# Optimization experiments

Measured on AMD Instinct MI355X. Metric: run time of the kernel, lower is better.

Reference implementation:

```python
import jax, jax.numpy as jnp
import numpy as np

B, C, L = 16, 256, 4096
P, Q = 100, 20


def setup_inputs() -> dict:
    key = jax.random.key(0)
    k1, k2, k3, k4 = jax.random.split(key, 4)
    X = jax.random.normal(k1, (B, C, L), dtype=jnp.float32)
    projections = jax.random.normal(k2, (P, C), dtype=jnp.float32)
    # min < max per projection. Projected values ~ N(0, sqrt(C)), so scale ~ sqrt(C).
    scale = jnp.sqrt(jnp.float32(C))
    min_vals = -scale * (1.0 + jax.random.uniform(k3, (P,), dtype=jnp.float32))
    max_vals = scale * (1.0 + jax.random.uniform(k4, (P,), dtype=jnp.float32))
    return {"X": X, "projections": projections, "min_vals": min_vals, "max_vals": max_vals}


def reference(X, projections, min_vals, max_vals):
    # conv1d with kernel size 1 == per-position projection: [B,C,L] x [P,C] -> [B,P,L]
    a = jnp.einsum('bcl,pc->bpl', X, projections)
    # all quantile thresholds at once: thr[p,q] = min + (max-min)*(q+1)/(Q+1)
    fracs = (jnp.arange(1, Q + 1, dtype=jnp.float32)) / jnp.float32(Q + 1)  # [Q]
    thr = min_vals[:, None] + (max_vals - min_vals)[:, None] * fracs[None, :]  # [P,Q]
    # set[b,p,l,q] = a[b,p,l] < thr[p,q]
    set_ = (a[:, :, :, None] < thr[None, :, None, :]).astype(jnp.float32)  # [B,P,L,Q]
    cdf = jnp.mean(set_, axis=2)  # [B,P,Q]
    # transpose(2,1) -> [B,L,P,Q]; reshape -> [B,L,P*Q]; transpose(2,1) -> [B,P*Q,L]
    set_out = jnp.transpose(set_, (0, 2, 1, 3)).reshape(B, L, P * Q)
    set_out = jnp.transpose(set_out, (0, 2, 1))  # [B, P*Q, L]
    cdf_out = cdf.reshape(B, P * Q)
    return (cdf_out, set_out)
```

## Files before the change

### kernel.cpp

```cpp
#include <hip/hip_runtime.h>

#define Bsz 16
#define Cc  256
#define Ll  4096
#define Pp  100
#define Qq  20
#define PQ  (Pp * Qq)

#define LTILE 1024
#define NLT   (Ll / LTILE)
#define GP    10
#define NPG   (Pp / GP)

typedef float f32x4 __attribute__((ext_vector_type(4)));

__global__ __launch_bounds__(256) void csf_main(
    const float* __restrict__ X,
    const float* __restrict__ proj,
    const float* __restrict__ mn,
    const float* __restrict__ mx,
    float* __restrict__ cdf,
    float* __restrict__ set_out) {
    const int lt  = blockIdx.x;
    const int pg  = blockIdx.y;
    const int b   = blockIdx.z;
    const int tid = threadIdx.x;
    const int l0  = lt * LTILE + tid * 4;
    const int p0  = __builtin_amdgcn_readfirstlane(pg * GP);

    const float* Xb = X + (size_t)b * Cc * Ll + l0;

    float acc[GP][4];
#pragma unroll
    for (int i = 0; i < GP; i++)
#pragma unroll
        for (int k = 0; k < 4; k++) acc[i][k] = 0.0f;

#pragma unroll 4
    for (int c = 0; c < Cc; c++) {
        const f32x4 x = *(const f32x4*)(Xb + (size_t)c * Ll);
#pragma unroll
        for (int i = 0; i < GP; i++) {
            const float w = proj[(size_t)(p0 + i) * Cc + c];
            acc[i][0] = __builtin_fmaf(x.x, w, acc[i][0]);
            acc[i][1] = __builtin_fmaf(x.y, w, acc[i][1]);
            acc[i][2] = __builtin_fmaf(x.z, w, acc[i][2]);
            acc[i][3] = __builtin_fmaf(x.w, w, acc[i][3]);
        }
    }

    float fr[Qq];
#pragma unroll
    for (int q = 0; q < Qq; q++) fr[q] = __fdiv_rn((float)(q + 1), 21.0f);

    float* ob = set_out + (size_t)b * PQ * Ll + l0;
    const bool lane0 = ((tid & 63) == 0);

#pragma unroll 1
    for (int i = 0; i < GP; i++) {
        const int p = p0 + i;
        const float mnp = mn[p];
        const float mxp = mx[p];
        const float d = __fsub_rn(mxp, mnp);
#pragma unroll
        for (int q = 0; q < Qq; q++) {
            const float thr = __fadd_rn(mnp, __fmul_rn(d, fr[q]));
            const bool b0 = acc[i][0] < thr;
            const bool b1 = acc[i][1] < thr;
            const bool b2 = acc[i][2] < thr;
            const bool b3 = acc[i][3] < thr;
            f32x4 o;
            o.x = b0 ? 1.0f : 0.0f;
            o.y = b1 ? 1.0f : 0.0f;
            o.z = b2 ? 1.0f : 0.0f;
            o.w = b3 ? 1.0f : 0.0f;
            __builtin_nontemporal_store(o, (f32x4*)(ob + (size_t)(p * Qq + q) * Ll));
            const int cnt = __popcll(__ballot(b0)) + __popcll(__ballot(b1))
                          + __popcll(__ballot(b2)) + __popcll(__ballot(b3));
            if (lane0) {
                atomicAdd(&cdf[(size_t)b * PQ + p * Qq + q],
                          (float)cnt * (1.0f / (float)Ll));
            }
        }
    }
}

extern "C" void kernel_launch(void* const* d_in, const int* in_sizes, int n_in,
                              void* d_out, int out_size, void* d_ws, size_t ws_size,
                              hipStream_t stream) {
    const float* X    = (const float*)d_in[0];
    const float* proj = (const float*)d_in[1];
    const float* mn   = (const float*)d_in[2];
    const float* mx   = (const float*)d_in[3];

    float* cdf     = (float*)d_out;
    float* set_out = cdf + (size_t)Bsz * PQ;

    (void)hipMemsetAsync(cdf, 0, (size_t)Bsz * PQ * sizeof(float), stream);

    dim3 grid(NLT, NPG, Bsz);
    csf_main<<<grid, 256, 0, stream>>>(X, proj, mn, mx, cdf, set_out);
}
```

Baseline: 606.4 us.

## Split projection and thresholding into two kernels, staging projections in output buffer

Projection now runs in its own kernel where each thread keeps all 100 projection accumulators and reads X exactly once, with 8-channel software prefetch. The old kernel re-read X once per group of 10 projections. The projected values go to the first quantile slot of the output, and a second kernel reads them back to write the thresholded masks and cdf. In exchange it adds an extra round trip through global memory, a second launch, and high register pressure from the 100 accumulators, which may lower occupancy or cause spills.

```diff
diff --git a/kernel.cpp b/kernel.cpp
--- a/kernel.cpp
+++ b/kernel.cpp
@@ -7,97 +7,113 @@
 #define Qq  20
 #define PQ  (Pp * Qq)
 
-#define LTILE 1024
-#define NLT   (Ll / LTILE)
-#define GP    10
-#define NPG   (Pp / GP)
-
 typedef float f32x4 __attribute__((ext_vector_type(4)));
 
-__global__ __launch_bounds__(256) void csf_main(
+
+__global__ __launch_bounds__(256) void csf_proj(
     const float* __restrict__ X,
     const float* __restrict__ proj,
+    float* __restrict__ set_out) {
+  const int l = blockIdx.x * 256 + threadIdx.x;
+  const int b = blockIdx.y;
+  const float* Xb = X + (size_t)b * Cc * Ll + l;
+
+  float acc[Pp];
+#pragma unroll
+  for (int p = 0; p < Pp; p++) acc[p] = 0.0f;
+
+  float x[8];
+#pragma unroll
+  for (int j = 0; j < 8; j++) x[j] = Xb[(size_t)j * Ll];
+
+#pragma unroll 1
+  for (int cc = 0; cc < Cc; cc += 8) {
+    float xn[8];
+    const bool more = (cc + 8 < Cc);
+    if (more) {
+#pragma unroll
+      for (int j = 0; j < 8; j++) xn[j] = Xb[(size_t)(cc + 8 + j) * Ll];
+    }
+#pragma unroll
+    for (int p = 0; p < Pp; p++) {
+      const float* pr = proj + (size_t)p * Cc + cc;
+#pragma unroll
+      for (int j = 0; j < 8; j++)
+        acc[p] = __builtin_fmaf(x[j], pr[j], acc[p]);
+    }
+    if (more) {
+#pragma unroll
+      for (int j = 0; j < 8; j++) x[j] = xn[j];
+    }
+  }
+
+  float* ob = set_out + (size_t)b * PQ * Ll + l;
+#pragma unroll
+  for (int p = 0; p < Pp; p++)
+    ob[(size_t)p * Qq * Ll] = acc[p];
+}
+
+__global__ __launch_bounds__(256) void csf_thresh(
     const float* __restrict__ mn,
     const float* __restrict__ mx,
     float* __restrict__ cdf,
     float* __restrict__ set_out) {
-    const int lt  = blockIdx.x;
-    const int pg  = blockIdx.y;
-    const int b   = blockIdx.z;
-    const int tid = threadIdx.x;
-    const int l0  = lt * LTILE + tid * 4;
-    const int p0  = __builtin_amdgcn_readfirstlane(pg * GP);
+  const int lt  = blockIdx.x;
+  const int p   = blockIdx.y;
+  const int b   = blockIdx.z;
+  const int tid = threadIdx.x;
+  const int l0  = lt * 1024 + tid * 4;
 
-    const float* Xb = X + (size_t)b * Cc * Ll + l0;
+  float* ob = set_out + (size_t)b * PQ * Ll + (size_t)p * Qq * Ll + l0;
+  const f32x4 a = *(const f32x4*)ob;
 
-    float acc[GP][4];
+  const float mnp = mn[p];
+  const float mxp = mx[p];
+  const float d   = __fsub_rn(mxp, mnp);
+
+  const float FR[Qq] = {
+     1.0f/21.0f,  2.0f/21.0f,  3.0f/21.0f,  4.0f/21.0f,  5.0f/21.0f,
+     6.0f/21.0f,  7.0f/21.0f,  8.0f/21.0f,  9.0f/21.0f, 10.0f/21.0f,
+    11.0f/21.0f, 12.0f/21.0f, 13.0f/21.0f, 14.0f/21.0f, 15.0f/21.0f,
+    16.0f/21.0f, 17.0f/21.0f, 18.0f/21.0f, 19.0f/21.0f, 20.0f/21.0f };
+
+  const bool lane0 = ((tid & 63) == 0);
+  float* cp = cdf + (size_t)b * PQ + (size_t)p * Qq;
+
 #pragma unroll
-    for (int i = 0; i < GP; i++)
-#pragma unroll
-        for (int k = 0; k < 4; k++) acc[i][k] = 0.0f;
-
-#pragma unroll 4
-    for (int c = 0; c < Cc; c++) {
-        const f32x4 x = *(const f32x4*)(Xb + (size_t)c * Ll);
-#pragma unroll
-        for (int i = 0; i < GP; i++) {
-            const float w = proj[(size_t)(p0 + i) * Cc + c];
-            acc[i][0] = __builtin_fmaf(x.x, w, acc[i][0]);
-            acc[i][1] = __builtin_fmaf(x.y, w, acc[i][1]);
-            acc[i][2] = __builtin_fmaf(x.z, w, acc[i][2]);
-            acc[i][3] = __builtin_fmaf(x.w, w, acc[i][3]);
-        }
+  for (int q = 0; q < Qq; q++) {
+    const float thr = __fadd_rn(mnp, __fmul_rn(d, FR[q]));
+    const bool b0 = a.x < thr;
+    const bool b1 = a.y < thr;
+    const bool b2 = a.z < thr;
+    const bool b3 = a.w < thr;
+    f32x4 o;
+    o.x = b0 ? 1.0f : 0.0f;
+    o.y = b1 ? 1.0f : 0.0f;
+    o.z = b2 ? 1.0f : 0.0f;
+    o.w = b3 ? 1.0f : 0.0f;
+    __builtin_nontemporal_store(o, (f32x4*)(ob + (size_t)q * Ll));
+    const int cnt = __popcll(__ballot(b0)) + __popcll(__ballot(b1))
+                  + __popcll(__ballot(b2)) + __popcll(__ballot(b3));
+    if (lane0) {
+      atomicAdd(cp + q, (float)cnt * (1.0f / (float)Ll));
     }
-
-    float fr[Qq];
-#pragma unroll
-    for (int q = 0; q < Qq; q++) fr[q] = __fdiv_rn((float)(q + 1), 21.0f);
-
-    float* ob = set_out + (size_t)b * PQ * Ll + l0;
-    const bool lane0 = ((tid & 63) == 0);
-
-#pragma unroll 1
-    for (int i = 0; i < GP; i++) {
-        const int p = p0 + i;
-        const float mnp = mn[p];
-        const float mxp = mx[p];
-        const float d = __fsub_rn(mxp, mnp);
-#pragma unroll
-        for (int q = 0; q < Qq; q++) {
-            const float thr = __fadd_rn(mnp, __fmul_rn(d, fr[q]));
-            const bool b0 = acc[i][0] < thr;
-            const bool b1 = acc[i][1] < thr;
-            const bool b2 = acc[i][2] < thr;
-            const bool b3 = acc[i][3] < thr;
-            f32x4 o;
-            o.x = b0 ? 1.0f : 0.0f;
-            o.y = b1 ? 1.0f : 0.0f;
-            o.z = b2 ? 1.0f : 0.0f;
-            o.w = b3 ? 1.0f : 0.0f;
-            __builtin_nontemporal_store(o, (f32x4*)(ob + (size_t)(p * Qq + q) * Ll));
-            const int cnt = __popcll(__ballot(b0)) + __popcll(__ballot(b1))
-                          + __popcll(__ballot(b2)) + __popcll(__ballot(b3));
-            if (lane0) {
-                atomicAdd(&cdf[(size_t)b * PQ + p * Qq + q],
-                          (float)cnt * (1.0f / (float)Ll));
-            }
-        }
-    }
+  }
 }
 
 extern "C" void kernel_launch(void* const* d_in, const int* in_sizes, int n_in,
                               void* d_out, int out_size, void* d_ws, size_t ws_size,
                               hipStream_t stream) {
-    const float* X    = (const float*)d_in[0];
-    const float* proj = (const float*)d_in[1];
-    const float* mn   = (const float*)d_in[2];
-    const float* mx   = (const float*)d_in[3];
+  const float* X    = (const float*)d_in[0];
+  const float* proj = (const float*)d_in[1];
+  const float* mn   = (const float*)d_in[2];
+  const float* mx   = (const float*)d_in[3];
 
-    float* cdf     = (float*)d_out;
-    float* set_out = cdf + (size_t)Bsz * PQ;
+  float* cdf     = (float*)d_out;
+  float* set_out = cdf + (size_t)Bsz * PQ;
 
-    (void)hipMemsetAsync(cdf, 0, (size_t)Bsz * PQ * sizeof(float), stream);
+  (void)hipMemsetAsync(cdf, 0, (size_t)Bsz * PQ * sizeof(float), stream);
 
-    dim3 grid(NLT, NPG, Bsz);
-    csf_main<<<grid, 256, 0, stream>>>(X, proj, mn, mx, cdf, set_out);
+  csf_proj<<<dim3(Ll / 256, Bsz), 256, 0, stream>>>(X, proj, set_out);
+  csf_thresh<<<dim3(Ll / 1024, Pp, Bsz), 256, 0, stream>>>(mn, mx, cdf, set_out);
 }
```

Result: slower. 871.7 us (+43.7%).

## Stage X tiles in shared memory and split projections across waves per block

Applied to the files above, without the earlier changes.

The kernel now handles one batch and a 64-position tile per block, staging 64-channel chunks of X in LDS. Each of its four waves computes 25 projections for all 64 positions, so X is read from global memory once rather than ten times across projection groups. Each lane now holds one position instead of four. Stores therefore become scalar (4-byte) nontemporal writes, and there are four times as many ballots and atomics per output element. The output write of roughly 524 MB dominates, so the narrower stores could hurt write efficiency.

```diff
diff --git a/kernel.cpp b/kernel.cpp
--- a/kernel.cpp
+++ b/kernel.cpp
@@ -7,97 +7,95 @@
 #define Qq  20
 #define PQ  (Pp * Qq)
 
-#define LTILE 1024
-#define NLT   (Ll / LTILE)
-#define GP    10
-#define NPG   (Pp / GP)
+#define LT   64
+#define CCH  64
+#define PW   25
 
 typedef float f32x4 __attribute__((ext_vector_type(4)));
 
-__global__ __launch_bounds__(256) void csf_main(
+__global__ __launch_bounds__(256, 4) void csf_fused(
     const float* __restrict__ X,
     const float* __restrict__ proj,
     const float* __restrict__ mn,
     const float* __restrict__ mx,
     float* __restrict__ cdf,
     float* __restrict__ set_out) {
-    const int lt  = blockIdx.x;
-    const int pg  = blockIdx.y;
-    const int b   = blockIdx.z;
-    const int tid = threadIdx.x;
-    const int l0  = lt * LTILE + tid * 4;
-    const int p0  = __builtin_amdgcn_readfirstlane(pg * GP);
+  __shared__ float xs[CCH][LT];
 
-    const float* Xb = X + (size_t)b * Cc * Ll + l0;
+  const int b    = blockIdx.y;
+  const int l0   = blockIdx.x * LT;
+  const int tid  = threadIdx.x;
+  const int wave = tid >> 6;
+  const int lane = tid & 63;
+  const int p0   = __builtin_amdgcn_readfirstlane(wave * PW);
 
-    float acc[GP][4];
+  const int lsub = (tid & 15) * 4;
+  const int crow = tid >> 4;
+  const float* Xg = X + (size_t)b * Cc * Ll + l0 + lsub;
+
+  float acc[PW];
 #pragma unroll
-    for (int i = 0; i < GP; i++)
-#pragma unroll
-        for (int k = 0; k < 4; k++) acc[i][k] = 0.0f;
-
-#pragma unroll 4
-    for (int c = 0; c < Cc; c++) {
-        const f32x4 x = *(const f32x4*)(Xb + (size_t)c * Ll);
-#pragma unroll
-        for (int i = 0; i < GP; i++) {
-            const float w = proj[(size_t)(p0 + i) * Cc + c];
-            acc[i][0] = __builtin_fmaf(x.x, w, acc[i][0]);
-            acc[i][1] = __builtin_fmaf(x.y, w, acc[i][1]);
-            acc[i][2] = __builtin_fmaf(x.z, w, acc[i][2]);
-            acc[i][3] = __builtin_fmaf(x.w, w, acc[i][3]);
-        }
-    }
-
-    float fr[Qq];
-#pragma unroll
-    for (int q = 0; q < Qq; q++) fr[q] = __fdiv_rn((float)(q + 1), 21.0f);
-
-    float* ob = set_out + (size_t)b * PQ * Ll + l0;
-    const bool lane0 = ((tid & 63) == 0);
+  for (int i = 0; i < PW; i++) acc[i] = 0.0f;
 
 #pragma unroll 1
-    for (int i = 0; i < GP; i++) {
-        const int p = p0 + i;
-        const float mnp = mn[p];
-        const float mxp = mx[p];
-        const float d = __fsub_rn(mxp, mnp);
+  for (int ch = 0; ch < Cc; ch += CCH) {
+    if (ch) __syncthreads();
 #pragma unroll
-        for (int q = 0; q < Qq; q++) {
-            const float thr = __fadd_rn(mnp, __fmul_rn(d, fr[q]));
-            const bool b0 = acc[i][0] < thr;
-            const bool b1 = acc[i][1] < thr;
-            const bool b2 = acc[i][2] < thr;
-            const bool b3 = acc[i][3] < thr;
-            f32x4 o;
-            o.x = b0 ? 1.0f : 0.0f;
-            o.y = b1 ? 1.0f : 0.0f;
-            o.z = b2 ? 1.0f : 0.0f;
-            o.w = b3 ? 1.0f : 0.0f;
-            __builtin_nontemporal_store(o, (f32x4*)(ob + (size_t)(p * Qq + q) * Ll));
-            const int cnt = __popcll(__ballot(b0)) + __popcll(__ballot(b1))
-                          + __popcll(__ballot(b2)) + __popcll(__ballot(b3));
-            if (lane0) {
-                atomicAdd(&cdf[(size_t)b * PQ + p * Qq + q],
-                          (float)cnt * (1.0f / (float)Ll));
-            }
-        }
+    for (int cc = 0; cc < CCH; cc += 16) {
+      *(f32x4*)&xs[cc + crow][lsub] =
+          *(const f32x4*)(Xg + (size_t)(ch + cc + crow) * Ll);
     }
+    __syncthreads();
+#pragma unroll 4
+    for (int c = 0; c < CCH; c++) {
+      const float x = xs[c][lane];
+#pragma unroll
+      for (int i = 0; i < PW; i++)
+        acc[i] = __builtin_fmaf(x, proj[(size_t)(p0 + i) * Cc + ch + c], acc[i]);
+    }
+  }
+
+  const float FR[Qq] = {
+     1.0f/21.0f,  2.0f/21.0f,  3.0f/21.0f,  4.0f/21.0f,  5.0f/21.0f,
+     6.0f/21.0f,  7.0f/21.0f,  8.0f/21.0f,  9.0f/21.0f, 10.0f/21.0f,
+    11.0f/21.0f, 12.0f/21.0f, 13.0f/21.0f, 14.0f/21.0f, 15.0f/21.0f,
+    16.0f/21.0f, 17.0f/21.0f, 18.0f/21.0f, 19.0f/21.0f, 20.0f/21.0f };
+
+  float* ob = set_out + (size_t)b * PQ * Ll + l0 + lane;
+  float* cb = cdf + (size_t)b * PQ;
+  const bool lane0 = (lane == 0);
+
+#pragma unroll 1
+  for (int i = 0; i < PW; i++) {
+    const int p = p0 + i;
+    const float mnp = mn[p];
+    const float d   = __fsub_rn(mx[p], mnp);
+    float* obp = ob + (size_t)p * Qq * Ll;
+#pragma unroll
+    for (int q = 0; q < Qq; q++) {
+      const float thr = __fadd_rn(mnp, __fmul_rn(d, FR[q]));
+      const bool bb = acc[i] < thr;
+      __builtin_nontemporal_store(bb ? 1.0f : 0.0f, obp + (size_t)q * Ll);
+      const int cnt = __popcll(__ballot(bb));
+      if (lane0) {
+        atomicAdd(cb + (size_t)p * Qq + q, (float)cnt * (1.0f / (float)Ll));
+      }
+    }
+  }
 }
 
 extern "C" void kernel_launch(void* const* d_in, const int* in_sizes, int n_in,
                               void* d_out, int out_size, void* d_ws, size_t ws_size,
                               hipStream_t stream) {
-    const float* X    = (const float*)d_in[0];
-    const float* proj = (const float*)d_in[1];
-    const float* mn   = (const float*)d_in[2];
-    const float* mx   = (const float*)d_in[3];
+  const float* X    = (const float*)d_in[0];
+  const float* proj = (const float*)d_in[1];
+  const float* mn   = (const float*)d_in[2];
+  const float* mx   = (const float*)d_in[3];
 
-    float* cdf     = (float*)d_out;
-    float* set_out = cdf + (size_t)Bsz * PQ;
+  float* cdf     = (float*)d_out;
+  float* set_out = cdf + (size_t)Bsz * PQ;
 
-    (void)hipMemsetAsync(cdf, 0, (size_t)Bsz * PQ * sizeof(float), stream);
+  (void)hipMemsetAsync(cdf, 0, (size_t)Bsz * PQ * sizeof(float), stream);
 
-    dim3 grid(NLT, NPG, Bsz);
-    csf_main<<<grid, 256, 0, stream>>>(X, proj, mn, mx, cdf, set_out);
+  csf_fused<<<dim3(Ll / LT, Bsz), 256, 0, stream>>>(X, proj, mn, mx, cdf, set_out);
 }
```

Result: slower. 755.0 us (+24.5%).

## Restructure projection tiling: 25 projections per wave, prefetched X chunks, q-outer thresholding

Applied to the files above, without the earlier changes.

Each wave now computes 25 projections over 256 L positions, so every X load is reused across more projections and X is re-read only twice per batch instead of ten times. The channel loop is blocked by 8 with register double-buffering of the next X chunk to overlap loads with FMAs. The threshold/store phase is reordered q-outer, so each lane issues 25 streaming stores per q, and lane 0 issues the 25 cdf atomics in a batch. The cost is much higher register pressure (100 accumulators plus prefetch buffers) and fewer threads per block, which lowers occupancy. The kernel time is probably dominated by the ~525 MB write of the set output anyway.

```diff
diff --git a/kernel.cpp b/kernel.cpp
--- a/kernel.cpp
+++ b/kernel.cpp
@@ -7,97 +7,122 @@
 #define Qq  20
 #define PQ  (Pp * Qq)
 
-#define LTILE 1024
-#define NLT   (Ll / LTILE)
-#define GP    10
-#define NPG   (Pp / GP)
+#define PW   25
+#define LT   256
+#define CG   8
+#define NPG  2
 
 typedef float f32x4 __attribute__((ext_vector_type(4)));
 
-__global__ __launch_bounds__(256) void csf_main(
+__global__ __launch_bounds__(128, 1) void csf_fused(
     const float* __restrict__ X,
     const float* __restrict__ proj,
     const float* __restrict__ mn,
     const float* __restrict__ mx,
     float* __restrict__ cdf,
     float* __restrict__ set_out) {
-    const int lt  = blockIdx.x;
-    const int pg  = blockIdx.y;
-    const int b   = blockIdx.z;
-    const int tid = threadIdx.x;
-    const int l0  = lt * LTILE + tid * 4;
-    const int p0  = __builtin_amdgcn_readfirstlane(pg * GP);
+  const int lt   = blockIdx.x;
+  const int pg   = blockIdx.y;
+  const int b    = blockIdx.z;
+  const int tid  = threadIdx.x;
+  const int wave = tid >> 6;
+  const int lane = tid & 63;
+  const int l0   = lt * LT + lane * 4;
+  const int p0   = __builtin_amdgcn_readfirstlane(pg * (2 * PW) + wave * PW);
 
-    const float* Xb = X + (size_t)b * Cc * Ll + l0;
+  const float* Xb = X + (size_t)b * Cc * Ll + l0;
 
-    float acc[GP][4];
+  float acc[PW][4];
 #pragma unroll
-    for (int i = 0; i < GP; i++)
+  for (int i = 0; i < PW; i++)
 #pragma unroll
-        for (int k = 0; k < 4; k++) acc[i][k] = 0.0f;
+    for (int k = 0; k < 4; k++) acc[i][k] = 0.0f;
 
-#pragma unroll 4
-    for (int c = 0; c < Cc; c++) {
-        const f32x4 x = *(const f32x4*)(Xb + (size_t)c * Ll);
+  f32x4 xv[CG];
 #pragma unroll
-        for (int i = 0; i < GP; i++) {
-            const float w = proj[(size_t)(p0 + i) * Cc + c];
-            acc[i][0] = __builtin_fmaf(x.x, w, acc[i][0]);
-            acc[i][1] = __builtin_fmaf(x.y, w, acc[i][1]);
-            acc[i][2] = __builtin_fmaf(x.z, w, acc[i][2]);
-            acc[i][3] = __builtin_fmaf(x.w, w, acc[i][3]);
-        }
-    }
-
-    float fr[Qq];
-#pragma unroll
-    for (int q = 0; q < Qq; q++) fr[q] = __fdiv_rn((float)(q + 1), 21.0f);
-
-    float* ob = set_out + (size_t)b * PQ * Ll + l0;
-    const bool lane0 = ((tid & 63) == 0);
+  for (int j = 0; j < CG; j++) xv[j] = *(const f32x4*)(Xb + (size_t)j * Ll);
 
 #pragma unroll 1
-    for (int i = 0; i < GP; i++) {
-        const int p = p0 + i;
-        const float mnp = mn[p];
-        const float mxp = mx[p];
-        const float d = __fsub_rn(mxp, mnp);
+  for (int cc = 0; cc < Cc; cc += CG) {
+    f32x4 xn[CG];
+    const bool more = (cc + CG) < Cc;
+    if (more) {
 #pragma unroll
-        for (int q = 0; q < Qq; q++) {
-            const float thr = __fadd_rn(mnp, __fmul_rn(d, fr[q]));
-            const bool b0 = acc[i][0] < thr;
-            const bool b1 = acc[i][1] < thr;
-            const bool b2 = acc[i][2] < thr;
-            const bool b3 = acc[i][3] < thr;
-            f32x4 o;
-            o.x = b0 ? 1.0f : 0.0f;
-            o.y = b1 ? 1.0f : 0.0f;
-            o.z = b2 ? 1.0f : 0.0f;
-            o.w = b3 ? 1.0f : 0.0f;
-            __builtin_nontemporal_store(o, (f32x4*)(ob + (size_t)(p * Qq + q) * Ll));
-            const int cnt = __popcll(__ballot(b0)) + __popcll(__ballot(b1))
-                          + __popcll(__ballot(b2)) + __popcll(__ballot(b3));
-            if (lane0) {
-                atomicAdd(&cdf[(size_t)b * PQ + p * Qq + q],
-                          (float)cnt * (1.0f / (float)Ll));
-            }
-        }
+      for (int j = 0; j < CG; j++)
+        xn[j] = *(const f32x4*)(Xb + (size_t)(cc + CG + j) * Ll);
     }
+#pragma unroll
+    for (int i = 0; i < PW; i++) {
+      const float* pr = proj + (size_t)(p0 + i) * Cc + cc;
+#pragma unroll
+      for (int j = 0; j < CG; j++) {
+        const float w = pr[j];
+        acc[i][0] = __builtin_fmaf(xv[j].x, w, acc[i][0]);
+        acc[i][1] = __builtin_fmaf(xv[j].y, w, acc[i][1]);
+        acc[i][2] = __builtin_fmaf(xv[j].z, w, acc[i][2]);
+        acc[i][3] = __builtin_fmaf(xv[j].w, w, acc[i][3]);
+      }
+    }
+    if (more) {
+#pragma unroll
+      for (int j = 0; j < CG; j++) xv[j] = xn[j];
+    }
+  }
+
+  float mnp[PW], dd[PW];
+#pragma unroll
+  for (int i = 0; i < PW; i++) {
+    mnp[i] = mn[p0 + i];
+    dd[i]  = __fsub_rn(mx[p0 + i], mnp[i]);
+  }
+
+  float* ob = set_out + (size_t)b * PQ * Ll + l0;
+  float* cb = cdf + (size_t)b * PQ + (size_t)p0 * Qq;
+  const bool lane0 = (lane == 0);
+
+#pragma unroll 1
+  for (int q = 0; q < Qq; q++) {
+    const float fr = __fdiv_rn((float)(q + 1), 21.0f);
+    int cnt[PW];
+#pragma unroll
+    for (int i = 0; i < PW; i++) {
+      const float thr = __fadd_rn(mnp[i], __fmul_rn(dd[i], fr));
+      const bool b0 = acc[i][0] < thr;
+      const bool b1 = acc[i][1] < thr;
+      const bool b2 = acc[i][2] < thr;
+      const bool b3 = acc[i][3] < thr;
+      f32x4 o;
+      o.x = b0 ? 1.0f : 0.0f;
+      o.y = b1 ? 1.0f : 0.0f;
+      o.z = b2 ? 1.0f : 0.0f;
+      o.w = b3 ? 1.0f : 0.0f;
+      __builtin_nontemporal_store(
+          o, (f32x4*)(ob + ((size_t)(p0 + i) * Qq + q) * Ll));
+      cnt[i] = __popcll(__ballot(b0)) + __popcll(__ballot(b1))
+             + __popcll(__ballot(b2)) + __popcll(__ballot(b3));
+    }
+    if (lane0) {
+#pragma unroll
+      for (int i = 0; i < PW; i++) {
+        atomicAdd(cb + (size_t)i * Qq + q, (float)cnt[i] * (1.0f / (float)Ll));
+      }
+    }
+  }
 }
 
 extern "C" void kernel_launch(void* const* d_in, const int* in_sizes, int n_in,
                               void* d_out, int out_size, void* d_ws, size_t ws_size,
                               hipStream_t stream) {
-    const float* X    = (const float*)d_in[0];
-    const float* proj = (const float*)d_in[1];
-    const float* mn   = (const float*)d_in[2];
-    const float* mx   = (const float*)d_in[3];
+  const float* X    = (const float*)d_in[0];
+  const float* proj = (const float*)d_in[1];
+  const float* mn   = (const float*)d_in[2];
+  const float* mx   = (const float*)d_in[3];
 
-    float* cdf     = (float*)d_out;
-    float* set_out = cdf + (size_t)Bsz * PQ;
+  float* cdf     = (float*)d_out;
+  float* set_out = cdf + (size_t)Bsz * PQ;
 
-    (void)hipMemsetAsync(cdf, 0, (size_t)Bsz * PQ * sizeof(float), stream);
+  (void)hipMemsetAsync(cdf, 0, (size_t)Bsz * PQ * sizeof(float), stream);
 
-    dim3 grid(NLT, NPG, Bsz);
-    csf_main<<<grid, 256, 0, stream>>>(X, proj, mn, mx, cdf, set_out);
+  csf_fused<<<dim3(Ll / LT, NPG, Bsz), 128, 0, stream>>>(X, proj, mn, mx, cdf,
+                                                         set_out);
 }
```

Result: slower. 727.6 us (+20.0%).
